# Performance work log

Measured on AMD Instinct MI355X. Metric: run time of the kernel, lower is better.

Reference implementation:

```python
import jax, jax.numpy as jnp
import numpy as np

H = 4  # attention heads (GCNFormer default)


def _ln(x, g, b, eps):
    mu = jnp.mean(x, -1, keepdims=True)
    var = jnp.mean((x - mu) ** 2, -1, keepdims=True)
    return (x - mu) / jnp.sqrt(var + eps) * g + b


def setup_inputs() -> dict:
    key = jax.random.key(0)
    ks = jax.random.split(key, 6)
    B, T, N, DIN, DE, HID, CS, OUT = 32, 12, 512, 3, 16, 64, 2, 12
    x = jax.random.normal(ks[0], (B, T, N, DIN), jnp.float32)
    node_emb = jax.random.normal(ks[1], (N, DE), jnp.float32)
    time_emb = jax.random.normal(ks[2], (B, T, DE), jnp.float32)
    wp = jax.random.normal(ks[3], (3, DE, 2, DIN + HID, HID), jnp.float32) * 0.1
    bp = jax.random.normal(ks[4], (3, DE, HID), jnp.float32) * 0.1
    gcn_ln_g = jnp.ones((3, DE), jnp.float32)
    gcn_ln_b = jnp.zeros((3, DE), jnp.float32)
    out_ln_g = jnp.ones((3, HID), jnp.float32)
    out_ln_b = jnp.zeros((3, HID), jnp.float32)
    pred_w = jax.random.normal(ks[5], (OUT, CS, HID), jnp.float32) * 0.1
    pred_b = jnp.zeros((OUT,), jnp.float32)
    return dict(x=x, node_emb=node_emb, time_emb=time_emb, wp=wp, bp=bp,
                gcn_ln_g=gcn_ln_g, gcn_ln_b=gcn_ln_b,
                out_ln_g=out_ln_g, out_ln_b=out_ln_b,
                pred_w=pred_w, pred_b=pred_b)


def reference(x, node_emb, time_emb, wp, bp, gcn_ln_g, gcn_ln_b,
              out_ln_g, out_ln_b, pred_w, pred_b):
    B, T, N, _ = x.shape
    HID = pred_w.shape[-1]
    hd = HID // H

    def gcnformer(xt, states, te_t, g):
        # GCN: learned dynamic adjacency from node+time embeddings
        emb = _ln(node_emb[None] + te_t[:, None], gcn_ln_g[g], gcn_ln_b[g], 1e-12)  # (B,N,DE)
        s2 = jax.nn.softmax(jnp.einsum('bnd,bmd->bnm', emb, emb), axis=-1)  # (B,N,N)
        xg2 = jnp.einsum('bnm,bmc->bnc', s2, xt)
        w = jnp.einsum('nd,dkio->nkio', node_emb, wp[g])  # (N,2,I,HID)
        gout = (jnp.einsum('bni,nio->bno', xt, w[:, 0])
                + jnp.einsum('bni,nio->bno', xg2, w[:, 1])
                + (te_t @ bp[g])[:, None])  # (B,N,HID)
        # attention: query = LN(gcn out), tgt_len=1; keys/values = past states
        q = _ln(gout, out_ln_g[g], out_ln_b[g], 1e-5)
        qh = q.reshape(B, N, H, hd)
        kh = states.reshape(B, N, -1, H, hd)  # (B,N,t,H,hd)
        score = jnp.einsum('bnhd,bnkhd->bnhk', qh, kh) / (hd ** 0.5)
        attn = jax.nn.softmax(score, axis=-1)
        o = jnp.einsum('bnhk,bnkhd->bnhd', attn, kh).reshape(B, N, HID)
        return gout + o  # residual; dropout is identity in eval

    def gru_step(xt, states, te_t):
        state = states[:, :, -1]
        ias = jnp.concatenate([xt, state], -1)
        z = jax.nn.sigmoid(gcnformer(ias, states, te_t, 0))
        r = jax.nn.sigmoid(gcnformer(ias, states, te_t, 1))
        cand = jnp.concatenate([xt, z * state], -1)
        hc = jnp.tanh(gcnformer(cand, states, te_t, 2))
        return r * state + (1.0 - r) * hc

    h0 = jnp.zeros((B, N, HID), x.dtype)
    hs = [h0]
    for t in range(T):  # recurrence with growing attention context (as in torch)
        states = jnp.stack(hs, axis=2)  # (B,N,t+1,HID)
        hs.append(gru_step(x[:, t], states, time_emb[:, t]))
    cur = jnp.stack(hs[1:], axis=1)  # (B,T,N,HID)
    CS = pred_w.shape[1]
    inp = cur[:, -CS:]  # (B,CS,N,HID)
    # Conv2d(CS, out_steps, kernel=(1,HID)) == einsum over (channel, hidden)
    pred = jnp.einsum('bcnh,och->bon', inp, pred_w) + pred_b[None, :, None]
    return pred[..., None]  # (B,out_steps,N,1)
```

## Files before the change

### kernel.cpp

```cpp
#include <hip/hip_runtime.h>
#include <math.h>

#define Bv   32
#define Tv   12
#define Nv   512
#define DINv 3
#define DEv  16
#define HIDv 64
#define INXv 67
#define CSv  2
#define OUTv 12
#define WSZ  (2 * INXv * HIDv)

typedef __attribute__((ext_vector_type(8))) short bf16x8;
typedef __attribute__((ext_vector_type(4))) float f32x4;

__device__ __forceinline__ float sigmoidf_(float x) { return 1.0f / (1.0f + __expf(-x)); }

__device__ __forceinline__ unsigned short f2bf(float f) {
  unsigned u = __float_as_uint(f);
  unsigned r = (u + 0x7FFFu + ((u >> 16) & 1u)) >> 16;
  return (unsigned short)r;
}
__device__ __forceinline__ float bf2f(unsigned short h) {
  return __uint_as_float(((unsigned)h) << 16);
}

__global__ __launch_bounds__(384) void k_emb(const float* __restrict__ node_emb,
                                             const float* __restrict__ te,
                                             const float* __restrict__ lng,
                                             const float* __restrict__ lnb,
                                             unsigned short* __restrict__ embp) {
  const int t = blockIdx.y, b = blockIdx.z;
  const int g = threadIdx.x >> 7;
  const int nl = threadIdx.x & 127;
  const int n = blockIdx.x * 128 + nl;
  float v[16];
  float mu = 0.f;
#pragma unroll
  for (int d = 0; d < 16; ++d) {
    v[d] = node_emb[n * 16 + d] + te[(b * Tv + t) * 16 + d];
    mu += v[d];
  }
  mu *= 0.0625f;
  float var = 0.f;
#pragma unroll
  for (int d = 0; d < 16; ++d) { const float c = v[d] - mu; var += c * c; }
  var *= 0.0625f;
  const float rs = rsqrtf(var + 1e-12f);
  unsigned short hi[16], lo[16];
#pragma unroll
  for (int d = 0; d < 16; ++d) {
    const float e = (v[d] - mu) * rs * lng[g * 16 + d] + lnb[g * 16 + d];
    hi[d] = f2bf(e);
    lo[d] = f2bf(e - bf2f(hi[d]));
  }
  unsigned w[16];
#pragma unroll
  for (int d = 0; d < 8; ++d) {
    w[d] = (unsigned)hi[2 * d] | ((unsigned)hi[2 * d + 1] << 16);
    w[8 + d] = (unsigned)lo[2 * d] | ((unsigned)lo[2 * d + 1] << 16);
  }
  uint4* op = (uint4*)(embp + ((((size_t)g * Tv + t) * Bv + b) * Nv + n) * 32);
  op[0] = make_uint4(w[0], w[1], w[2], w[3]);
  op[1] = make_uint4(w[4], w[5], w[6], w[7]);
  op[2] = make_uint4(w[8], w[9], w[10], w[11]);
  op[3] = make_uint4(w[12], w[13], w[14], w[15]);
}

__global__ __launch_bounds__(256) void k_wpre(const float* __restrict__ node_emb,
                                              const float* __restrict__ wp,
                                              float* __restrict__ W) {
  const int g = blockIdx.y;
  const int j = blockIdx.x * 256 + threadIdx.x;
  const int n0 = blockIdx.z * 128;
  if (j >= WSZ) return;
  const float* wpg = wp + (size_t)g * (DEv * WSZ);
  float wr[16];
#pragma unroll
  for (int d = 0; d < 16; ++d) wr[d] = wpg[(size_t)d * WSZ + j];
  float* Wg = W + (size_t)g * Nv * WSZ;
  for (int n = n0; n < n0 + 128; ++n) {
    const float4 e0 = *(const float4*)(node_emb + n * 16);
    const float4 e1 = *(const float4*)(node_emb + n * 16 + 4);
    const float4 e2 = *(const float4*)(node_emb + n * 16 + 8);
    const float4 e3 = *(const float4*)(node_emb + n * 16 + 12);
    float s = e0.x * wr[0] + e0.y * wr[1] + e0.z * wr[2] + e0.w * wr[3]
            + e1.x * wr[4] + e1.y * wr[5] + e1.z * wr[6] + e1.w * wr[7]
            + e2.x * wr[8] + e2.y * wr[9] + e2.z * wr[10] + e2.w * wr[11]
            + e3.x * wr[12] + e3.y * wr[13] + e3.z * wr[14] + e3.w * wr[15];
    Wg[(size_t)n * WSZ + j] = s;
  }
}

__global__ __launch_bounds__(64) void k_tb(const float* __restrict__ te,
                                           const float* __restrict__ bp,
                                           float* __restrict__ TB) {
  const int g = blockIdx.y;
  const int bt = blockIdx.x;
  const int b = bt / Tv, t = bt % Tv;
  const int o = threadIdx.x;
  float s = 0.f;
#pragma unroll
  for (int d = 0; d < DEv; ++d) s += te[(b * Tv + t) * DEv + d] * bp[(g * DEv + d) * HIDv + o];
  TB[(((size_t)g * Bv + b) * Tv + t) * HIDv + o] = s;
}

__global__ __launch_bounds__(256) void k_vprep(const float* __restrict__ src,
                                               const float* __restrict__ x,
                                               unsigned short* __restrict__ Vs,
                                               int t) {
  const int b = blockIdx.y;
  const int m0 = blockIdx.x * 128;
  const int tid = threadIdx.x;
  __shared__ float sl[128][69];
  const float* srcb = src + ((size_t)b * Nv + m0) * HIDv;
  for (int j = tid; j < 2048; j += 256) {
    const int r = j >> 4, c4 = j & 15;
    const float4 v = *(const float4*)(srcb + r * HIDv + c4 * 4);
    sl[r][c4 * 4 + 0] = v.x; sl[r][c4 * 4 + 1] = v.y;
    sl[r][c4 * 4 + 2] = v.z; sl[r][c4 * 4 + 3] = v.w;
  }
  const float* xb = x + (((size_t)b * Tv + t) * Nv + m0) * DINv;
  for (int j = tid; j < 384; j += 256) sl[j / 3][64 + j % 3] = xb[j];
  __syncthreads();
  unsigned short* VsB = Vs + (size_t)b * 2 * 80 * 512;
  for (int j = tid; j < 80 * 128; j += 256) {
    const int m = j & 127, c = j >> 7;
    const float v = (c < 67) ? sl[m][c] : 0.f;
    const unsigned short h = f2bf(v);
    VsB[(size_t)c * 512 + m0 + m] = h;
    VsB[(size_t)(80 + c) * 512 + m0 + m] = f2bf(v - bf2f(h));
  }
}

__global__ __launch_bounds__(256) void k_gatt(const unsigned short* __restrict__ embp,
                                              const unsigned short* __restrict__ Vs,
                                              float* __restrict__ xg2,
                                              int t, int g0) {
  const int z = blockIdx.z, g = g0 + z;
  const int b = blockIdx.y;
  const int n0 = blockIdx.x * 64;
  const int tid = threadIdx.x;
  const int w = tid >> 6, lane = tid & 63;
  const int l15 = lane & 15, g4 = lane >> 4;

  __shared__ unsigned short vh[80][40];
  __shared__ unsigned short vl[80][40];
  __shared__ unsigned short ph_[4][16][40];
  __shared__ unsigned short pl_[4][16][40];

  const unsigned short* embB = embp + ((((size_t)g * Tv + t) * Bv + b) * Nv) * 32;
  const unsigned short* VsB = Vs + (size_t)b * 2 * 80 * 512;

  const int qrow = n0 + w * 16 + l15;
  const bf16x8 qhi = *(const bf16x8*)(embB + (size_t)qrow * 32 + (g4 & 1) * 8);
  const bf16x8 qlo = *(const bf16x8*)(embB + (size_t)qrow * 32 + 16 + (g4 & 1) * 8);

  f32x4 acc[5];
#pragma unroll
  for (int i = 0; i < 5; ++i) acc[i] = (f32x4){0.f, 0.f, 0.f, 0.f};
  float dn[4] = {0.f, 0.f, 0.f, 0.f};

  for (int m0 = 0; m0 < Nv; m0 += 32) {
    __syncthreads();
    for (int j = tid; j < 640; j += 256) {
      const int chunk = j & 3, r = j >> 2;
      const int c = (r >= 80) ? r - 80 : r;
      const uint4 v = *(const uint4*)(VsB + (size_t)r * 512 + m0 + chunk * 8);
      if (r >= 80) *(uint4*)&vl[c][chunk * 8] = v;
      else         *(uint4*)&vh[c][chunk * 8] = v;
    }
    __syncthreads();

    const bf16x8 eb0 = *(const bf16x8*)(embB + (size_t)(m0 + l15) * 32 + g4 * 8);
    const bf16x8 eb1 = *(const bf16x8*)(embB + (size_t)(m0 + 16 + l15) * 32 + g4 * 8);
    f32x4 s0 = (f32x4){0.f, 0.f, 0.f, 0.f};
    f32x4 s1 = (f32x4){0.f, 0.f, 0.f, 0.f};
    s0 = __builtin_amdgcn_mfma_f32_16x16x32_bf16(qhi, eb0, s0, 0, 0, 0);
    s0 = __builtin_amdgcn_mfma_f32_16x16x32_bf16(qlo, eb0, s0, 0, 0, 0);
    s1 = __builtin_amdgcn_mfma_f32_16x16x32_bf16(qhi, eb1, s1, 0, 0, 0);
    s1 = __builtin_amdgcn_mfma_f32_16x16x32_bf16(qlo, eb1, s1, 0, 0, 0);

#pragma unroll
    for (int j = 0; j < 4; ++j) {
      const float p0 = __expf(s0[j] - 16.f);
      const float p1 = __expf(s1[j] - 16.f);
      dn[j] += p0 + p1;
      const int r = g4 * 4 + j;
      const unsigned short h0 = f2bf(p0), h1 = f2bf(p1);
      ph_[w][r][l15] = h0;      pl_[w][r][l15] = f2bf(p0 - bf2f(h0));
      ph_[w][r][16 + l15] = h1; pl_[w][r][16 + l15] = f2bf(p1 - bf2f(h1));
    }
    const bf16x8 pAh = *(const bf16x8*)&ph_[w][l15][g4 * 8];
    const bf16x8 pAl = *(const bf16x8*)&pl_[w][l15][g4 * 8];

#pragma unroll
    for (int tl = 0; tl < 5; ++tl) {
      const bf16x8 vhf = *(const bf16x8*)&vh[tl * 16 + l15][g4 * 8];
      const bf16x8 vlf = *(const bf16x8*)&vl[tl * 16 + l15][g4 * 8];
      acc[tl] = __builtin_amdgcn_mfma_f32_16x16x32_bf16(pAh, vhf, acc[tl], 0, 0, 0);
      acc[tl] = __builtin_amdgcn_mfma_f32_16x16x32_bf16(pAh, vlf, acc[tl], 0, 0, 0);
      acc[tl] = __builtin_amdgcn_mfma_f32_16x16x32_bf16(pAl, vhf, acc[tl], 0, 0, 0);
    }
  }
#pragma unroll
  for (int j = 0; j < 4; ++j) {
    dn[j] += __shfl_xor(dn[j], 1);
    dn[j] += __shfl_xor(dn[j], 2);
    dn[j] += __shfl_xor(dn[j], 4);
    dn[j] += __shfl_xor(dn[j], 8);
  }
  float* outB = xg2 + (((size_t)z * Bv + b) * Nv) * 80;
#pragma unroll
  for (int j = 0; j < 4; ++j) {
    const float r = 1.f / dn[j];
    const int n = n0 + w * 16 + g4 * 4 + j;
#pragma unroll
    for (int tl = 0; tl < 5; ++tl) {
      const int c = tl * 16 + l15;
      if (c < 67) outB[(size_t)n * 80 + c] = acc[tl][j] * r;
    }
  }
}

__global__ __launch_bounds__(256) void k_k2(const float* __restrict__ x,
                                            const float* __restrict__ Wb,
                                            const float* __restrict__ TB,
                                            const float* __restrict__ oln_g,
                                            const float* __restrict__ oln_b,
                                            const float* __restrict__ xg2,
                                            const float* __restrict__ srcst,
                                            const float* __restrict__ states,
                                            const float* __restrict__ stcur,
                                            float* __restrict__ zs,
                                            float* __restrict__ rb,
                                            float* __restrict__ hnew,
                                            int t, int g0) {
  const int zb = blockIdx.z;
  const int g = g0 + zb;
  const int n = blockIdx.x;
  __shared__ float xts[INXv][36];
  __shared__ float g2s[INXv][36];
  const int tid = threadIdx.x;

  {
    const int bq = tid >> 3, cc = tid & 7;
    const float* sp = &srcst[((size_t)bq * Nv + n) * HIDv + cc * 8];
    const float4 a = *(const float4*)sp;
    const float4 c = *(const float4*)(sp + 4);
    xts[3 + cc * 8 + 0][bq] = a.x; xts[3 + cc * 8 + 1][bq] = a.y;
    xts[3 + cc * 8 + 2][bq] = a.z; xts[3 + cc * 8 + 3][bq] = a.w;
    xts[3 + cc * 8 + 4][bq] = c.x; xts[3 + cc * 8 + 5][bq] = c.y;
    xts[3 + cc * 8 + 6][bq] = c.z; xts[3 + cc * 8 + 7][bq] = c.w;
    const float* gp = &xg2[(((size_t)zb * Bv + bq) * Nv + n) * 80 + cc * 8];
    const float4 p = *(const float4*)gp;
    const float4 r2 = *(const float4*)(gp + 4);
    g2s[3 + cc * 8 + 0][bq] = p.x;  g2s[3 + cc * 8 + 1][bq] = p.y;
    g2s[3 + cc * 8 + 2][bq] = p.z;  g2s[3 + cc * 8 + 3][bq] = p.w;
    g2s[3 + cc * 8 + 4][bq] = r2.x; g2s[3 + cc * 8 + 5][bq] = r2.y;
    g2s[3 + cc * 8 + 6][bq] = r2.z; g2s[3 + cc * 8 + 7][bq] = r2.w;
  }
  if (tid < Bv) {
    const int bq = tid;
    const float* xp = &x[(((size_t)bq * Tv + t) * Nv + n) * DINv];
    xts[0][bq] = xp[0]; xts[1][bq] = xp[1]; xts[2][bq] = xp[2];
    const float* gp = &xg2[(((size_t)zb * Bv + bq) * Nv + n) * 80 + 64];
    g2s[0][bq] = gp[0]; g2s[1][bq] = gp[1]; g2s[2][bq] = gp[2];
  }
  __syncthreads();

  const int o = tid & 63, bg = tid >> 6;
  const float* W0 = Wb + ((size_t)g * Nv + n) * WSZ + o;
  const float* W1 = W0 + INXv * HIDv;
  float acc[8] = {0, 0, 0, 0, 0, 0, 0, 0};
  for (int i = 0; i < INXv; ++i) {
    const float w0 = W0[i * HIDv];
    const float w1 = W1[i * HIDv];
    const float4 xa = *(const float4*)&xts[i][bg * 8];
    const float4 xc = *(const float4*)&xts[i][bg * 8 + 4];
    const float4 ga = *(const float4*)&g2s[i][bg * 8];
    const float4 gc = *(const float4*)&g2s[i][bg * 8 + 4];
    acc[0] += xa.x * w0 + ga.x * w1; acc[1] += xa.y * w0 + ga.y * w1;
    acc[2] += xa.z * w0 + ga.z * w1; acc[3] += xa.w * w0 + ga.w * w1;
    acc[4] += xc.x * w0 + gc.x * w1; acc[5] += xc.y * w0 + gc.y * w1;
    acc[6] += xc.z * w0 + gc.z * w1; acc[7] += xc.w * w0 + gc.w * w1;
  }
#pragma unroll
  for (int u = 0; u < 8; ++u)
    acc[u] += TB[(((size_t)g * Bv + bg * 8 + u) * Tv + t) * HIDv + o];

  const float gg = oln_g[g * HIDv + o], bb = oln_b[g * HIDv + o];
  float q[8];
#pragma unroll
  for (int u = 0; u < 8; ++u) {
    float s = acc[u];
    s += __shfl_xor(s, 1);  s += __shfl_xor(s, 2);  s += __shfl_xor(s, 4);
    s += __shfl_xor(s, 8);  s += __shfl_xor(s, 16); s += __shfl_xor(s, 32);
    const float mu = s * (1.f / 64.f);
    const float c = acc[u] - mu;
    float v = c * c;
    v += __shfl_xor(v, 1);  v += __shfl_xor(v, 2);  v += __shfl_xor(v, 4);
    v += __shfl_xor(v, 8);  v += __shfl_xor(v, 16); v += __shfl_xor(v, 32);
    const float rs = rsqrtf(v * (1.f / 64.f) + 1e-5f);
    q[u] = c * rs * gg + bb;
  }

  float oa[8] = {0, 0, 0, 0, 0, 0, 0, 0};
  float den[8] = {0, 0, 0, 0, 0, 0, 0, 0};
  for (int k = 0; k <= t; ++k) {
#pragma unroll
    for (int u = 0; u < 8; ++u) {
      const float kv = states[(((size_t)k * Bv + bg * 8 + u) * Nv + n) * HIDv + o];
      float sc = q[u] * kv;
      sc += __shfl_xor(sc, 1); sc += __shfl_xor(sc, 2);
      sc += __shfl_xor(sc, 4); sc += __shfl_xor(sc, 8);
      const float p = __expf(sc * 0.25f);
      den[u] += p;
      oa[u] += p * kv;
    }
  }
  float pre[8];
#pragma unroll
  for (int u = 0; u < 8; ++u) pre[u] = acc[u] + oa[u] / den[u];

  if (g == 0) {
#pragma unroll
    for (int u = 0; u < 8; ++u) {
      const size_t off = ((size_t)(bg * 8 + u) * Nv + n) * HIDv + o;
      zs[off] = sigmoidf_(pre[u]) * stcur[off];
    }
  } else if (g == 1) {
#pragma unroll
    for (int u = 0; u < 8; ++u) {
      const size_t off = ((size_t)(bg * 8 + u) * Nv + n) * HIDv + o;
      rb[off] = sigmoidf_(pre[u]);
    }
  } else {
#pragma unroll
    for (int u = 0; u < 8; ++u) {
      const size_t off = ((size_t)(bg * 8 + u) * Nv + n) * HIDv + o;
      const float r = rb[off];
      hnew[off] = r * stcur[off] + (1.f - r) * tanhf(pre[u]);
    }
  }
}

__global__ __launch_bounds__(256) void k_pred(const float* __restrict__ states,
                                              const float* __restrict__ pw,
                                              const float* __restrict__ pb,
                                              float* __restrict__ out) {
  __shared__ float pws[OUTv * CSv * HIDv];
  __shared__ float pbs[OUTv];
  const int tid = threadIdx.x;
  for (int j = tid; j < OUTv * CSv * HIDv; j += 256) pws[j] = pw[j];
  if (tid < OUTv) pbs[tid] = pb[tid];
  __syncthreads();
  const int n = blockIdx.x * 256 + tid;
  const int b = blockIdx.y;
  const float* s0p = &states[(((size_t)(Tv - 1) * Bv + b) * Nv + n) * HIDv];
  const float* s1p = &states[(((size_t)Tv * Bv + b) * Nv + n) * HIDv];
  float4 va[16], vb[16];
#pragma unroll
  for (int j = 0; j < 16; ++j) {
    va[j] = *(const float4*)&s0p[j * 4];
    vb[j] = *(const float4*)&s1p[j * 4];
  }
#pragma unroll
  for (int oo = 0; oo < OUTv; ++oo) {
    float acc = pbs[oo];
    const float* w0 = &pws[(oo * CSv + 0) * HIDv];
    const float* w1 = &pws[(oo * CSv + 1) * HIDv];
#pragma unroll
    for (int j = 0; j < 16; ++j) {
      acc += va[j].x * w0[j * 4 + 0] + va[j].y * w0[j * 4 + 1] +
             va[j].z * w0[j * 4 + 2] + va[j].w * w0[j * 4 + 3];
      acc += vb[j].x * w1[j * 4 + 0] + vb[j].y * w1[j * 4 + 1] +
             vb[j].z * w1[j * 4 + 2] + vb[j].w * w1[j * 4 + 3];
    }
    out[((size_t)b * OUTv + oo) * Nv + n] = acc;
  }
}

extern "C" void kernel_launch(void* const* d_in, const int* in_sizes, int n_in,
                              void* d_out, int out_size, void* d_ws, size_t ws_size,
                              hipStream_t stream) {
  (void)in_sizes; (void)n_in; (void)out_size; (void)ws_size;
  const float* x        = (const float*)d_in[0];
  const float* node_emb = (const float*)d_in[1];
  const float* time_emb = (const float*)d_in[2];
  const float* wp       = (const float*)d_in[3];
  const float* bp       = (const float*)d_in[4];
  const float* gcn_g    = (const float*)d_in[5];
  const float* gcn_b    = (const float*)d_in[6];
  const float* out_g    = (const float*)d_in[7];
  const float* out_b    = (const float*)d_in[8];
  const float* pred_w   = (const float*)d_in[9];
  const float* pred_b   = (const float*)d_in[10];

  float* ws = (float*)d_ws;
  float* W    = ws;
  float* TB   = W   + (size_t)3 * Nv * WSZ;
  float* ST   = TB  + (size_t)3 * Bv * Tv * HIDv;
  float* XG   = ST  + (size_t)(Tv + 1) * Bv * Nv * HIDv;
  float* ZS   = XG  + (size_t)2 * Bv * Nv * 80;
  float* RB   = ZS  + (size_t)Bv * Nv * HIDv;
  unsigned short* EMBp = (unsigned short*)(RB + (size_t)Bv * Nv * HIDv);
  unsigned short* Vs   = EMBp + (size_t)3 * Tv * Bv * Nv * 32;

  hipMemsetAsync(ST, 0, (size_t)Bv * Nv * HIDv * sizeof(float), stream);
  k_emb<<<dim3(Nv / 128, Tv, Bv), 384, 0, stream>>>(node_emb, time_emb, gcn_g, gcn_b, EMBp);
  k_wpre<<<dim3(34, 3, 4), 256, 0, stream>>>(node_emb, wp, W);
  k_tb<<<dim3(Bv * Tv, 3), 64, 0, stream>>>(time_emb, bp, TB);

  for (int t = 0; t < Tv; ++t) {
    float* st_t  = ST + (size_t)t * Bv * Nv * HIDv;
    float* st_t1 = st_t + (size_t)Bv * Nv * HIDv;
    k_vprep<<<dim3(4, Bv), 256, 0, stream>>>(st_t, x, Vs, t);
    k_gatt<<<dim3(Nv / 64, Bv, 2), 256, 0, stream>>>(EMBp, Vs, XG, t, 0);
    k_k2<<<dim3(Nv, 1, 2), 256, 0, stream>>>(x, W, TB, out_g, out_b, XG,
                                             st_t, ST, st_t, ZS, RB, st_t1, t, 0);
    k_vprep<<<dim3(4, Bv), 256, 0, stream>>>(ZS, x, Vs, t);
    k_gatt<<<dim3(Nv / 64, Bv, 1), 256, 0, stream>>>(EMBp, Vs, XG, t, 2);
    k_k2<<<dim3(Nv, 1, 1), 256, 0, stream>>>(x, W, TB, out_g, out_b, XG,
                                             ZS, ST, st_t, ZS, RB, st_t1, t, 2);
  }
  k_pred<<<dim3(Nv / 256, Bv), 256, 0, stream>>>(ST, pred_w, pred_b, (float*)d_out);
}
```

Before: 1.736 ms.

## Fuse bf16 split V-prep into k_k2 epilogue, split gatt over key halves

Removes the per-step k_vprep kernels. k_k2 now writes the hi/lo bf16 transposed state planes directly in its epilogue, and the x part of V is precomputed once for all timesteps. k_gatt splits the key dimension into two halves, and each half writes an unnormalized partial plus its denominator, which doubles grid parallelism. k_k2 merges the two halves and normalizes. k_k2 also moves to 512 threads and handles both z/r gates in one block so the srcst staging is shared. The cost is extra partial-sum memory traffic and scattered bf16 stores, strided by n, in the k_k2 epilogue.

```diff
diff --git a/kernel.cpp b/kernel.cpp
--- a/kernel.cpp
+++ b/kernel.cpp
@@ -106,39 +106,31 @@
   TB[(((size_t)g * Bv + b) * Tv + t) * HIDv + o] = s;
 }
 
-__global__ __launch_bounds__(256) void k_vprep(const float* __restrict__ src,
-                                               const float* __restrict__ x,
-                                               unsigned short* __restrict__ Vs,
-                                               int t) {
-  const int b = blockIdx.y;
-  const int m0 = blockIdx.x * 128;
+__global__ __launch_bounds__(256) void k_xprep(const float* __restrict__ x,
+                                               unsigned short* __restrict__ Xs) {
+  const int t = blockIdx.x, b = blockIdx.y;
   const int tid = threadIdx.x;
-  __shared__ float sl[128][69];
-  const float* srcb = src + ((size_t)b * Nv + m0) * HIDv;
-  for (int j = tid; j < 2048; j += 256) {
-    const int r = j >> 4, c4 = j & 15;
-    const float4 v = *(const float4*)(srcb + r * HIDv + c4 * 4);
-    sl[r][c4 * 4 + 0] = v.x; sl[r][c4 * 4 + 1] = v.y;
-    sl[r][c4 * 4 + 2] = v.z; sl[r][c4 * 4 + 3] = v.w;
-  }
-  const float* xb = x + (((size_t)b * Tv + t) * Nv + m0) * DINv;
-  for (int j = tid; j < 384; j += 256) sl[j / 3][64 + j % 3] = xb[j];
+  __shared__ float sl[1536];
+  const float* xb = x + ((size_t)b * Tv + t) * (Nv * 3);
+  for (int j = tid; j < 1536; j += 256) sl[j] = xb[j];
   __syncthreads();
-  unsigned short* VsB = Vs + (size_t)b * 2 * 80 * 512;
-  for (int j = tid; j < 80 * 128; j += 256) {
-    const int m = j & 127, c = j >> 7;
-    const float v = (c < 67) ? sl[m][c] : 0.f;
+  unsigned short* XB = Xs + ((size_t)t * Bv + b) * (2 * 3 * 512);
+  for (int j = tid; j < 1536; j += 256) {
+    const int ci = j >> 9, m = j & 511;
+    const float v = sl[m * 3 + ci];
     const unsigned short h = f2bf(v);
-    VsB[(size_t)c * 512 + m0 + m] = h;
-    VsB[(size_t)(80 + c) * 512 + m0 + m] = f2bf(v - bf2f(h));
+    XB[(size_t)ci * 512 + m] = h;
+    XB[(size_t)(3 + ci) * 512 + m] = f2bf(v - bf2f(h));
   }
 }
 
 __global__ __launch_bounds__(256) void k_gatt(const unsigned short* __restrict__ embp,
                                               const unsigned short* __restrict__ Vs,
+                                              const unsigned short* __restrict__ Xs,
                                               float* __restrict__ xg2,
                                               int t, int g0) {
-  const int z = blockIdx.z, g = g0 + z;
+  const int bz = blockIdx.z, z = bz >> 1, mh = bz & 1;
+  const int g = g0 + z;
   const int b = blockIdx.y;
   const int n0 = blockIdx.x * 64;
   const int tid = threadIdx.x;
@@ -150,8 +142,14 @@
   __shared__ unsigned short ph_[4][16][40];
   __shared__ unsigned short pl_[4][16][40];
 
+  for (int i = tid; i < 13 * 40; i += 256) {
+    vh[67 + i / 40][i % 40] = 0;
+    vl[67 + i / 40][i % 40] = 0;
+  }
+
   const unsigned short* embB = embp + ((((size_t)g * Tv + t) * Bv + b) * Nv) * 32;
-  const unsigned short* VsB = Vs + (size_t)b * 2 * 80 * 512;
+  const unsigned short* VsB = Vs + (size_t)b * 128 * 512;
+  const unsigned short* XsB = Xs + ((size_t)t * Bv + b) * (6 * 512);
 
   const int qrow = n0 + w * 16 + l15;
   const bf16x8 qhi = *(const bf16x8*)(embB + (size_t)qrow * 32 + (g4 & 1) * 8);
@@ -162,14 +160,24 @@
   for (int i = 0; i < 5; ++i) acc[i] = (f32x4){0.f, 0.f, 0.f, 0.f};
   float dn[4] = {0.f, 0.f, 0.f, 0.f};
 
-  for (int m0 = 0; m0 < Nv; m0 += 32) {
+  const int mbase = mh * 256;
+  for (int m0 = mbase; m0 < mbase + 256; m0 += 32) {
     __syncthreads();
-    for (int j = tid; j < 640; j += 256) {
-      const int chunk = j & 3, r = j >> 2;
-      const int c = (r >= 80) ? r - 80 : r;
-      const uint4 v = *(const uint4*)(VsB + (size_t)r * 512 + m0 + chunk * 8);
-      if (r >= 80) *(uint4*)&vl[c][chunk * 8] = v;
-      else         *(uint4*)&vh[c][chunk * 8] = v;
+    for (int j = tid; j < 536; j += 256) {
+      if (j < 512) {
+        const int r = j >> 2, ch = j & 3;
+        const int c = r & 63, plane = r >> 6;
+        const uint4 v = *(const uint4*)(VsB + (size_t)r * 512 + m0 + ch * 8);
+        if (plane) *(uint4*)&vl[c][ch * 8] = v;
+        else       *(uint4*)&vh[c][ch * 8] = v;
+      } else {
+        const int j2 = j - 512;
+        const int r2 = j2 >> 2, ch = j2 & 3;
+        const int ci = r2 % 3, plane = r2 / 3;
+        const uint4 v = *(const uint4*)(XsB + (size_t)r2 * 512 + m0 + ch * 8);
+        if (plane) *(uint4*)&vl[64 + ci][ch * 8] = v;
+        else       *(uint4*)&vh[64 + ci][ch * 8] = v;
+      }
     }
     __syncthreads();
 
@@ -211,20 +219,21 @@
     dn[j] += __shfl_xor(dn[j], 4);
     dn[j] += __shfl_xor(dn[j], 8);
   }
-  float* outB = xg2 + (((size_t)z * Bv + b) * Nv) * 80;
+  float* outB = xg2 + ((((size_t)z * 2 + mh) * Bv + b) * Nv) * 80;
 #pragma unroll
   for (int j = 0; j < 4; ++j) {
-    const float r = 1.f / dn[j];
     const int n = n0 + w * 16 + g4 * 4 + j;
 #pragma unroll
     for (int tl = 0; tl < 5; ++tl) {
       const int c = tl * 16 + l15;
-      if (c < 67) outB[(size_t)n * 80 + c] = acc[tl][j] * r;
-    }
-  }
-}
-
-__global__ __launch_bounds__(256) void k_k2(const float* __restrict__ x,
+      if (c < 67) outB[(size_t)n * 80 + c] = acc[tl][j];
+    }
+    if (l15 == 0) outB[(size_t)n * 80 + 72] = dn[j];
+  }
+}
+
+template <int NG>
+__global__ __launch_bounds__(512) void k_k2(const float* __restrict__ x,
                                             const float* __restrict__ Wb,
                                             const float* __restrict__ TB,
                                             const float* __restrict__ oln_g,
@@ -236,15 +245,21 @@
                                             float* __restrict__ zs,
                                             float* __restrict__ rb,
                                             float* __restrict__ hnew,
+                                            unsigned short* __restrict__ Vout,
                                             int t, int g0) {
-  const int zb = blockIdx.z;
-  const int g = g0 + zb;
   const int n = blockIdx.x;
+  const int tid = threadIdx.x;
   __shared__ float xts[INXv][36];
-  __shared__ float g2s[INXv][36];
-  const int tid = threadIdx.x;
-
-  {
+  __shared__ float g2s[NG][INXv][36];
+  __shared__ float rden_s[NG][32];
+
+  if (tid < NG * 32) {
+    const int gz2 = tid >> 5, bq = tid & 31;
+    const size_t base = ((((size_t)gz2 * 2) * Bv + bq) * Nv + n) * 80;
+    const float d = xg2[base + 72] + xg2[base + (size_t)Bv * Nv * 80 + 72];
+    rden_s[gz2][bq] = 1.f / d;
+  }
+  if (tid < 256) {
     const int bq = tid >> 3, cc = tid & 7;
     const float* sp = &srcst[((size_t)bq * Nv + n) * HIDv + cc * 8];
     const float4 a = *(const float4*)sp;
@@ -253,47 +268,75 @@
     xts[3 + cc * 8 + 2][bq] = a.z; xts[3 + cc * 8 + 3][bq] = a.w;
     xts[3 + cc * 8 + 4][bq] = c.x; xts[3 + cc * 8 + 5][bq] = c.y;
     xts[3 + cc * 8 + 6][bq] = c.z; xts[3 + cc * 8 + 7][bq] = c.w;
-    const float* gp = &xg2[(((size_t)zb * Bv + bq) * Nv + n) * 80 + cc * 8];
-    const float4 p = *(const float4*)gp;
-    const float4 r2 = *(const float4*)(gp + 4);
-    g2s[3 + cc * 8 + 0][bq] = p.x;  g2s[3 + cc * 8 + 1][bq] = p.y;
-    g2s[3 + cc * 8 + 2][bq] = p.z;  g2s[3 + cc * 8 + 3][bq] = p.w;
-    g2s[3 + cc * 8 + 4][bq] = r2.x; g2s[3 + cc * 8 + 5][bq] = r2.y;
-    g2s[3 + cc * 8 + 6][bq] = r2.z; g2s[3 + cc * 8 + 7][bq] = r2.w;
   }
   if (tid < Bv) {
-    const int bq = tid;
-    const float* xp = &x[(((size_t)bq * Tv + t) * Nv + n) * DINv];
-    xts[0][bq] = xp[0]; xts[1][bq] = xp[1]; xts[2][bq] = xp[2];
-    const float* gp = &xg2[(((size_t)zb * Bv + bq) * Nv + n) * 80 + 64];
-    g2s[0][bq] = gp[0]; g2s[1][bq] = gp[1]; g2s[2][bq] = gp[2];
+    const float* xp = &x[(((size_t)tid * Tv + t) * Nv + n) * DINv];
+    xts[0][tid] = xp[0]; xts[1][tid] = xp[1]; xts[2][tid] = xp[2];
   }
   __syncthreads();
 
-  const int o = tid & 63, bg = tid >> 6;
+  for (int j = tid; j < NG * 256; j += 512) {
+    const int gz2 = j >> 8, jj = j & 255;
+    const int bq = jj >> 3, cc = jj & 7;
+    const float rd = rden_s[gz2][bq];
+    const float* p0 = xg2 + ((((size_t)gz2 * 2 + 0) * Bv + bq) * Nv + n) * 80 + cc * 8;
+    const float* p1 = p0 + (size_t)Bv * Nv * 80;
+    const float4 a0 = *(const float4*)p0;
+    const float4 a1 = *(const float4*)(p0 + 4);
+    const float4 c0 = *(const float4*)p1;
+    const float4 c1 = *(const float4*)(p1 + 4);
+    g2s[gz2][3 + cc * 8 + 0][bq] = (a0.x + c0.x) * rd;
+    g2s[gz2][3 + cc * 8 + 1][bq] = (a0.y + c0.y) * rd;
+    g2s[gz2][3 + cc * 8 + 2][bq] = (a0.z + c0.z) * rd;
+    g2s[gz2][3 + cc * 8 + 3][bq] = (a0.w + c0.w) * rd;
+    g2s[gz2][3 + cc * 8 + 4][bq] = (a1.x + c1.x) * rd;
+    g2s[gz2][3 + cc * 8 + 5][bq] = (a1.y + c1.y) * rd;
+    g2s[gz2][3 + cc * 8 + 6][bq] = (a1.z + c1.z) * rd;
+    g2s[gz2][3 + cc * 8 + 7][bq] = (a1.w + c1.w) * rd;
+  }
+  for (int j = tid; j < NG * 96; j += 512) {
+    const int gz2 = j / 96, jj = j % 96;
+    const int bq = jj / 3, ci = jj % 3;
+    const float rd = rden_s[gz2][bq];
+    const size_t base = ((((size_t)gz2 * 2) * Bv + bq) * Nv + n) * 80 + 64 + ci;
+    g2s[gz2][ci][bq] = (xg2[base] + xg2[base + (size_t)Bv * Nv * 80]) * rd;
+  }
+  __syncthreads();
+
+  constexpr int NB = (NG == 2) ? 8 : 4;
+  const int gz = (NG == 2) ? (tid >> 8) : 0;
+  const int g = g0 + gz;
+  const int tl_ = (NG == 2) ? (tid & 255) : tid;
+  const int o = tl_ & 63;
+  const int bg = (NG == 2) ? ((tl_ >> 6) & 3) : (tl_ >> 6);
+  const int bb0 = bg * NB;
+
   const float* W0 = Wb + ((size_t)g * Nv + n) * WSZ + o;
   const float* W1 = W0 + INXv * HIDv;
-  float acc[8] = {0, 0, 0, 0, 0, 0, 0, 0};
+  float acc[NB];
+#pragma unroll
+  for (int u = 0; u < NB; ++u) acc[u] = 0.f;
   for (int i = 0; i < INXv; ++i) {
     const float w0 = W0[i * HIDv];
     const float w1 = W1[i * HIDv];
-    const float4 xa = *(const float4*)&xts[i][bg * 8];
-    const float4 xc = *(const float4*)&xts[i][bg * 8 + 4];
-    const float4 ga = *(const float4*)&g2s[i][bg * 8];
-    const float4 gc = *(const float4*)&g2s[i][bg * 8 + 4];
-    acc[0] += xa.x * w0 + ga.x * w1; acc[1] += xa.y * w0 + ga.y * w1;
-    acc[2] += xa.z * w0 + ga.z * w1; acc[3] += xa.w * w0 + ga.w * w1;
-    acc[4] += xc.x * w0 + gc.x * w1; acc[5] += xc.y * w0 + gc.y * w1;
-    acc[6] += xc.z * w0 + gc.z * w1; acc[7] += xc.w * w0 + gc.w * w1;
-  }
-#pragma unroll
-  for (int u = 0; u < 8; ++u)
-    acc[u] += TB[(((size_t)g * Bv + bg * 8 + u) * Tv + t) * HIDv + o];
+#pragma unroll
+    for (int u4 = 0; u4 < NB / 4; ++u4) {
+      const float4 xa = *(const float4*)&xts[i][bb0 + u4 * 4];
+      const float4 ga = *(const float4*)&g2s[gz][i][bb0 + u4 * 4];
+      acc[u4 * 4 + 0] += xa.x * w0 + ga.x * w1;
+      acc[u4 * 4 + 1] += xa.y * w0 + ga.y * w1;
+      acc[u4 * 4 + 2] += xa.z * w0 + ga.z * w1;
+      acc[u4 * 4 + 3] += xa.w * w0 + ga.w * w1;
+    }
+  }
+#pragma unroll
+  for (int u = 0; u < NB; ++u)
+    acc[u] += TB[(((size_t)g * Bv + bb0 + u) * Tv + t) * HIDv + o];
 
   const float gg = oln_g[g * HIDv + o], bb = oln_b[g * HIDv + o];
-  float q[8];
-#pragma unroll
-  for (int u = 0; u < 8; ++u) {
+  float q[NB];
+#pragma unroll
+  for (int u = 0; u < NB; ++u) {
     float s = acc[u];
     s += __shfl_xor(s, 1);  s += __shfl_xor(s, 2);  s += __shfl_xor(s, 4);
     s += __shfl_xor(s, 8);  s += __shfl_xor(s, 16); s += __shfl_xor(s, 32);
@@ -306,12 +349,13 @@
     q[u] = c * rs * gg + bb;
   }
 
-  float oa[8] = {0, 0, 0, 0, 0, 0, 0, 0};
-  float den[8] = {0, 0, 0, 0, 0, 0, 0, 0};
+  float oa[NB], den[NB];
+#pragma unroll
+  for (int u = 0; u < NB; ++u) { oa[u] = 0.f; den[u] = 0.f; }
   for (int k = 0; k <= t; ++k) {
 #pragma unroll
-    for (int u = 0; u < 8; ++u) {
-      const float kv = states[(((size_t)k * Bv + bg * 8 + u) * Nv + n) * HIDv + o];
+    for (int u = 0; u < NB; ++u) {
+      const float kv = states[(((size_t)k * Bv + bb0 + u) * Nv + n) * HIDv + o];
       float sc = q[u] * kv;
       sc += __shfl_xor(sc, 1); sc += __shfl_xor(sc, 2);
       sc += __shfl_xor(sc, 4); sc += __shfl_xor(sc, 8);
@@ -320,28 +364,38 @@
       oa[u] += p * kv;
     }
   }
-  float pre[8];
-#pragma unroll
-  for (int u = 0; u < 8; ++u) pre[u] = acc[u] + oa[u] / den[u];
+  float pre[NB];
+#pragma unroll
+  for (int u = 0; u < NB; ++u) pre[u] = acc[u] + oa[u] / den[u];
 
   if (g == 0) {
 #pragma unroll
-    for (int u = 0; u < 8; ++u) {
-      const size_t off = ((size_t)(bg * 8 + u) * Nv + n) * HIDv + o;
-      zs[off] = sigmoidf_(pre[u]) * stcur[off];
+    for (int u = 0; u < NB; ++u) {
+      const int bq = bb0 + u;
+      const size_t off = ((size_t)bq * Nv + n) * HIDv + o;
+      const float val = sigmoidf_(pre[u]) * stcur[off];
+      zs[off] = val;
+      const unsigned short h = f2bf(val);
+      Vout[((size_t)(bq * 2 + 0) * 64 + o) * 512 + n] = h;
+      Vout[((size_t)(bq * 2 + 1) * 64 + o) * 512 + n] = f2bf(val - bf2f(h));
     }
   } else if (g == 1) {
 #pragma unroll
-    for (int u = 0; u < 8; ++u) {
-      const size_t off = ((size_t)(bg * 8 + u) * Nv + n) * HIDv + o;
+    for (int u = 0; u < NB; ++u) {
+      const size_t off = ((size_t)(bb0 + u) * Nv + n) * HIDv + o;
       rb[off] = sigmoidf_(pre[u]);
     }
   } else {
 #pragma unroll
-    for (int u = 0; u < 8; ++u) {
-      const size_t off = ((size_t)(bg * 8 + u) * Nv + n) * HIDv + o;
+    for (int u = 0; u < NB; ++u) {
+      const int bq = bb0 + u;
+      const size_t off = ((size_t)bq * Nv + n) * HIDv + o;
       const float r = rb[off];
-      hnew[off] = r * stcur[off] + (1.f - r) * tanhf(pre[u]);
+      const float val = r * stcur[off] + (1.f - r) * tanhf(pre[u]);
+      hnew[off] = val;
+      const unsigned short h = f2bf(val);
+      Vout[((size_t)(bq * 2 + 0) * 64 + o) * 512 + n] = h;
+      Vout[((size_t)(bq * 2 + 1) * 64 + o) * 512 + n] = f2bf(val - bf2f(h));
     }
   }
 }
@@ -403,27 +457,29 @@
   float* TB   = W   + (size_t)3 * Nv * WSZ;
   float* ST   = TB  + (size_t)3 * Bv * Tv * HIDv;
   float* XG   = ST  + (size_t)(Tv + 1) * Bv * Nv * HIDv;
-  float* ZS   = XG  + (size_t)2 * Bv * Nv * 80;
+  float* ZS   = XG  + (size_t)4 * Bv * Nv * 80;
   float* RB   = ZS  + (size_t)Bv * Nv * HIDv;
   unsigned short* EMBp = (unsigned short*)(RB + (size_t)Bv * Nv * HIDv);
-  unsigned short* Vs   = EMBp + (size_t)3 * Tv * Bv * Nv * 32;
+  unsigned short* VsA  = EMBp + (size_t)3 * Tv * Bv * Nv * 32;
+  unsigned short* VsB  = VsA + (size_t)Bv * 128 * 512;
+  unsigned short* Xs   = VsB + (size_t)Bv * 128 * 512;
 
   hipMemsetAsync(ST, 0, (size_t)Bv * Nv * HIDv * sizeof(float), stream);
+  hipMemsetAsync(VsA, 0, (size_t)Bv * 128 * 512 * sizeof(unsigned short), stream);
   k_emb<<<dim3(Nv / 128, Tv, Bv), 384, 0, stream>>>(node_emb, time_emb, gcn_g, gcn_b, EMBp);
   k_wpre<<<dim3(34, 3, 4), 256, 0, stream>>>(node_emb, wp, W);
   k_tb<<<dim3(Bv * Tv, 3), 64, 0, stream>>>(time_emb, bp, TB);
+  k_xprep<<<dim3(Tv, Bv), 256, 0, stream>>>(x, Xs);
 
   for (int t = 0; t < Tv; ++t) {
     float* st_t  = ST + (size_t)t * Bv * Nv * HIDv;
     float* st_t1 = st_t + (size_t)Bv * Nv * HIDv;
-    k_vprep<<<dim3(4, Bv), 256, 0, stream>>>(st_t, x, Vs, t);
-    k_gatt<<<dim3(Nv / 64, Bv, 2), 256, 0, stream>>>(EMBp, Vs, XG, t, 0);
-    k_k2<<<dim3(Nv, 1, 2), 256, 0, stream>>>(x, W, TB, out_g, out_b, XG,
-                                             st_t, ST, st_t, ZS, RB, st_t1, t, 0);
-    k_vprep<<<dim3(4, Bv), 256, 0, stream>>>(ZS, x, Vs, t);
-    k_gatt<<<dim3(Nv / 64, Bv, 1), 256, 0, stream>>>(EMBp, Vs, XG, t, 2);
-    k_k2<<<dim3(Nv, 1, 1), 256, 0, stream>>>(x, W, TB, out_g, out_b, XG,
-                                             ZS, ST, st_t, ZS, RB, st_t1, t, 2);
+    k_gatt<<<dim3(Nv / 64, Bv, 4), 256, 0, stream>>>(EMBp, VsA, Xs, XG, t, 0);
+    k_k2<2><<<dim3(Nv), 512, 0, stream>>>(x, W, TB, out_g, out_b, XG,
+                                          st_t, ST, st_t, ZS, RB, st_t1, VsB, t, 0);
+    k_gatt<<<dim3(Nv / 64, Bv, 2), 256, 0, stream>>>(EMBp, VsB, Xs, XG, t, 2);
+    k_k2<1><<<dim3(Nv), 512, 0, stream>>>(x, W, TB, out_g, out_b, XG,
+                                          ZS, ST, st_t, ZS, RB, st_t1, VsA, t, 2);
   }
   k_pred<<<dim3(Nv / 256, Bv), 256, 0, stream>>>(ST, pred_w, pred_b, (float*)d_out);
 }
```

Measured after the change: 1.570 ms. 9.6% less time.
